# Kernel tuning notes

Measured on AMD Instinct MI355X. Metric: run time of the kernel, lower is better.

Reference implementation:

```python
import jax, jax.numpy as jnp
import numpy as np

B, S, D = 4, 4096, 1024
EPS_LN = 1e-5
EPS_REC = 1e-8


def _layernorm(x, g, b):
    mu = jnp.mean(x, axis=-1, keepdims=True)
    var = jnp.mean((x - mu) ** 2, axis=-1, keepdims=True)
    return (x - mu) * jax.lax.rsqrt(var + EPS_LN) * g + b


def setup_inputs() -> dict:
    key = jax.random.key(0)
    ks = jax.random.split(key, 8)
    scale = 1.0 / np.sqrt(D)
    return {
        "x": jax.random.normal(ks[0], (B, S, D), dtype=jnp.float32),
        "x_prev": jax.random.normal(ks[1], (B, S, D), dtype=jnp.float32),
        "mu": jnp.float32(0.5),
        "decay_w": jax.random.uniform(ks[2], (D, 1), jnp.float32, -scale, scale),
        "decay_b": jnp.zeros((1,), jnp.float32),
        "ln1_g": jnp.ones((D,), jnp.float32),
        "ln1_b": jnp.zeros((D,), jnp.float32),
        "Wr_w": jax.random.uniform(ks[3], (D, D), jnp.float32, -scale, scale),
        "Wr_b": jnp.zeros((D,), jnp.float32),
        "Wv_w": jax.random.uniform(ks[4], (D, D), jnp.float32, -scale, scale),
        "Wv_b": jnp.zeros((D,), jnp.float32),
        "ln2_g": jnp.ones((D,), jnp.float32),
        "ln2_b": jnp.zeros((D,), jnp.float32),
    }


def reference(x, x_prev, mu, decay_w, decay_b, ln1_g, ln1_b,
              Wr_w, Wr_b, Wv_w, Wv_b, ln2_g, ln2_b):
    # Shift (token-mix by scalar mu)
    shifted = mu * x + (1.0 - mu) * x_prev  # [B,S,D]

    # SequenceMergingSeq with C = V = W = shifted
    decay = jax.nn.sigmoid(jnp.einsum("bsd,do->bso", shifted, decay_w) + decay_b)  # [B,S,1]
    e = jnp.exp(shifted)                       # [B,S,D]
    ea = jnp.sum(e, axis=-1, keepdims=True)    # [B,S,1]
    ev = e * shifted                           # [B,S,D]

    def step(carry, inp):
        a, b = carry
        d_t, ea_t, ev_t = inp
        a = d_t * a + ea_t            # [B,1]
        b = d_t * b + ev_t            # [B,D]
        return (a, b), b / (a + EPS_REC)

    init = (jnp.zeros((B, 1), shifted.dtype), jnp.zeros((B, D), shifted.dtype))
    xs = (jnp.swapaxes(decay, 0, 1), jnp.swapaxes(ea, 0, 1), jnp.swapaxes(ev, 0, 1))
    _, out_sbd = jax.lax.scan(step, init, xs)  # [S,B,D]
    merged = _layernorm(jnp.swapaxes(out_sbd, 0, 1), ln1_g, ln1_b)  # [B,S,D]

    # StateCoupling
    gate = jax.nn.sigmoid(jnp.einsum("bsd,ed->bse", merged, Wr_w) + Wr_b)
    value = jnp.einsum("bsd,ed->bse", merged, Wv_w) + Wv_b
    coupled = _layernorm(gate * value, ln2_g, ln2_b)

    return shifted + coupled
```

## Files before the change

### kernel.cpp

```cpp
#include <hip/hip_runtime.h>

#define BATCH 4
#define SEQ   4096
#define DIM   1024
#define NCH   512
#define CHK   8
#define NROWS (BATCH*SEQ)
#define NKT   32

typedef __attribute__((ext_vector_type(4))) float f32x4;
typedef __attribute__((ext_vector_type(8))) short shortx8;
typedef __attribute__((ext_vector_type(4))) short shortx4;

static __device__ __forceinline__ unsigned short f2bf(float f){
    unsigned int u = __float_as_uint(f);
    u += 0x7FFFu + ((u >> 16) & 1u);
    return (unsigned short)(u >> 16);
}
static __device__ __forceinline__ float bf2f(unsigned short h){
    return __uint_as_float(((unsigned int)h) << 16);
}
static __device__ __forceinline__ float sigmoidf_fast(float x){
    return 1.0f / (1.0f + __expf(-x));
}
static __device__ __forceinline__ shortx4 pack4(f32x4 s){
    shortx4 o;
    o.x = (short)f2bf(s.x); o.y = (short)f2bf(s.y);
    o.z = (short)f2bf(s.z); o.w = (short)f2bf(s.w);
    return o;
}
static __device__ __forceinline__ f32x4 unpack4(shortx4 s){
    f32x4 o;
    o.x = bf2f((unsigned short)s.x); o.y = bf2f((unsigned short)s.y);
    o.z = bf2f((unsigned short)s.z); o.w = bf2f((unsigned short)s.w);
    return o;
}

__global__ __launch_bounds__(256) void k_shift_scan(
    const float* __restrict__ X, const float* __restrict__ XP,
    const float* __restrict__ mu_p, const float* __restrict__ dw,
    const float* __restrict__ db_p,
    const float* __restrict__ Wr, const float* __restrict__ Wv,
    unsigned short* __restrict__ Wcat,
    unsigned short* __restrict__ shifted,
    unsigned short* __restrict__ b_local, float* __restrict__ a_local,
    float* __restrict__ cumP)
{
    const int tid  = threadIdx.x;

    if (blockIdx.x >= 512){
        const int pb = blockIdx.x - 512;
        #pragma unroll 4
        for (int i = 0; i < 32; ++i){
            const int n = pb*32 + i;
            const int grp = n >> 5, r = n & 31;
            const float* src = (r < 16) ? (Wr + (size_t)(grp*16 + r)*DIM)
                                        : (Wv + (size_t)(grp*16 + (r-16))*DIM);
            f32x4 v = reinterpret_cast<const f32x4*>(src)[tid];
            reinterpret_cast<shortx4*>(Wcat)[n*256 + tid] = pack4(v);
        }
        return;
    }

    const int lane = tid & 63;
    const int wid  = tid >> 6;
    const int cid  = blockIdx.x*4 + wid;
    const int batch = cid >> 9;
    const int chunk = cid & (NCH-1);
    const int row0  = batch*SEQ + chunk*CHK;

    const float mu = mu_p[0];
    const float om = 1.0f - mu;
    const float db = db_p[0];

    const f32x4* dwv = reinterpret_cast<const f32x4*>(dw);
    const f32x4 w0 = dwv[lane], w1 = dwv[64+lane], w2 = dwv[128+lane], w3 = dwv[192+lane];

    f32x4 b0 = {0,0,0,0}, b1 = {0,0,0,0}, b2 = {0,0,0,0}, b3 = {0,0,0,0};
    float a_run = 0.f, cp = 1.f;

    const f32x4* Xv  = reinterpret_cast<const f32x4*>(X);
    const f32x4* XPv = reinterpret_cast<const f32x4*>(XP);
    shortx4* BL = reinterpret_cast<shortx4*>(b_local);
    shortx4* SH = reinterpret_cast<shortx4*>(shifted);

    for (int r = 0; r < CHK; ++r){
        const int row = row0 + r;
        const int rb  = row*(DIM/4);

        f32x4 x0 = Xv[rb+lane],     x1 = Xv[rb+64+lane],
              x2 = Xv[rb+128+lane], x3 = Xv[rb+192+lane];
        f32x4 p0 = XPv[rb+lane],     p1 = XPv[rb+64+lane],
              p2 = XPv[rb+128+lane], p3 = XPv[rb+192+lane];
        f32x4 s0 = mu*x0 + om*p0, s1 = mu*x1 + om*p1;
        f32x4 s2 = mu*x2 + om*p2, s3 = mu*x3 + om*p3;

        SH[rb+lane]     = pack4(s0);
        SH[rb+64+lane]  = pack4(s1);
        SH[rb+128+lane] = pack4(s2);
        SH[rb+192+lane] = pack4(s3);

        float dot = s0.x*w0.x + s0.y*w0.y + s0.z*w0.z + s0.w*w0.w
                  + s1.x*w1.x + s1.y*w1.y + s1.z*w1.z + s1.w*w1.w
                  + s2.x*w2.x + s2.y*w2.y + s2.z*w2.z + s2.w*w2.w
                  + s3.x*w3.x + s3.y*w3.y + s3.z*w3.z + s3.w*w3.w;

        f32x4 e0, e1, e2, e3;
        e0.x=__expf(s0.x); e0.y=__expf(s0.y); e0.z=__expf(s0.z); e0.w=__expf(s0.w);
        e1.x=__expf(s1.x); e1.y=__expf(s1.y); e1.z=__expf(s1.z); e1.w=__expf(s1.w);
        e2.x=__expf(s2.x); e2.y=__expf(s2.y); e2.z=__expf(s2.z); e2.w=__expf(s2.w);
        e3.x=__expf(s3.x); e3.y=__expf(s3.y); e3.z=__expf(s3.z); e3.w=__expf(s3.w);
        float ea = e0.x+e0.y+e0.z+e0.w + e1.x+e1.y+e1.z+e1.w
                 + e2.x+e2.y+e2.z+e2.w + e3.x+e3.y+e3.z+e3.w;

        #pragma unroll
        for (int off = 1; off < 64; off <<= 1){
            dot += __shfl_xor(dot, off, 64);
            ea  += __shfl_xor(ea,  off, 64);
        }

        const float dt = sigmoidf_fast(dot + db);
        a_run = dt*a_run + ea;
        cp   *= dt;
        b0 = dt*b0 + e0*s0;  b1 = dt*b1 + e1*s1;
        b2 = dt*b2 + e2*s2;  b3 = dt*b3 + e3*s3;

        BL[rb+lane]     = pack4(b0);
        BL[rb+64+lane]  = pack4(b1);
        BL[rb+128+lane] = pack4(b2);
        BL[rb+192+lane] = pack4(b3);
        if (lane == 0){ a_local[row] = a_run; cumP[row] = cp; }
    }
}

__global__ __launch_bounds__(64) void k_combine(
    const unsigned short* __restrict__ b_local, const float* __restrict__ a_local,
    const float* __restrict__ cumP,
    float* __restrict__ carryA, unsigned short* __restrict__ carryB)
{
    const int batch = blockIdx.x >> 2;
    const int dseg  = blockIdx.x & 3;
    const int tid = threadIdx.x;
    const int d0 = dseg*256 + tid*4;

    __shared__ float sP[NCH], sA[NCH];
    for (int c = tid; c < NCH; c += 64){
        const int er = batch*SEQ + c*CHK + (CHK-1);
        sP[c] = cumP[er];
        sA[c] = a_local[er];
    }
    __syncthreads();

    const unsigned short* bl = b_local + (size_t)batch*SEQ*DIM + d0;
    unsigned short* cB = carryB + (size_t)batch*NCH*DIM + d0;
    const bool wA = (dseg == 0 && tid == 0);
    float* cAp = carryA + batch*NCH;

    shortx4 pf[16];
    #pragma unroll
    for (int i = 0; i < 16; ++i)
        pf[i] = *reinterpret_cast<const shortx4*>(bl + (i*CHK + CHK-1)*DIM);

    f32x4 cb = {0,0,0,0};
    float ca = 0.f;

    for (int cc = 0; cc < NCH; cc += 16){
        const bool more = (cc + 16 < NCH);
        #pragma unroll
        for (int k = 0; k < 16; ++k){
            const int c = cc + k;
            f32x4 v = unpack4(pf[k]);
            if (more)
                pf[k] = *reinterpret_cast<const shortx4*>(bl + ((c+16)*CHK + CHK-1)*DIM);
            *reinterpret_cast<shortx4*>(cB + (size_t)c*DIM) = pack4(cb);
            if (wA) cAp[c] = ca;
            const float p = sP[c];
            cb = p*cb + v;
            ca = p*ca + sA[c];
        }
    }
}

__global__ __launch_bounds__(256) void k_fix_ln1(
    const unsigned short* __restrict__ b_local, const float* __restrict__ a_local,
    const float* __restrict__ cumP, const float* __restrict__ carryA,
    const unsigned short* __restrict__ carryB,
    const float* __restrict__ g1, const float* __restrict__ bb1,
    unsigned short* __restrict__ merged)
{
    const int tid = threadIdx.x, lane = tid & 63, wid = tid >> 6;
    const int row = blockIdx.x*4 + wid;
    const int batch = row >> 12;
    const int c = (row & (SEQ-1)) >> 3;

    const float cpv = cumP[row];
    const float a = a_local[row] + cpv * carryA[batch*NCH + c];
    const float inv_a = 1.0f / (a + 1e-8f);

    const shortx4* BL = reinterpret_cast<const shortx4*>(b_local) + (size_t)row*256;
    const shortx4* CB = reinterpret_cast<const shortx4*>(carryB) + (size_t)(batch*NCH + c)*256;

    f32x4 o[4];
    float s = 0.f, s2 = 0.f;
    #pragma unroll
    for (int j = 0; j < 4; ++j){
        f32x4 bl = unpack4(BL[j*64 + lane]);
        f32x4 cb = unpack4(CB[j*64 + lane]);
        f32x4 v = (bl + cpv*cb) * inv_a;
        o[j] = v;
        s  += v.x+v.y+v.z+v.w;
        s2 += v.x*v.x + v.y*v.y + v.z*v.z + v.w*v.w;
    }
    #pragma unroll
    for (int off = 1; off < 64; off <<= 1){
        s  += __shfl_xor(s,  off, 64);
        s2 += __shfl_xor(s2, off, 64);
    }
    const float mean = s * (1.0f/DIM);
    const float rstd = rsqrtf(s2*(1.0f/DIM) - mean*mean + 1e-5f);
    shortx4* MG = reinterpret_cast<shortx4*>(merged) + (size_t)row*256;
    #pragma unroll
    for (int j = 0; j < 4; ++j){
        f32x4 gg = reinterpret_cast<const f32x4*>(g1)[j*64 + lane];
        f32x4 bb = reinterpret_cast<const f32x4*>(bb1)[j*64 + lane];
        MG[j*64 + lane] = pack4((o[j] - mean)*rstd*gg + bb);
    }
}

typedef __attribute__((address_space(3))) unsigned int lds_uint;
typedef __attribute__((address_space(1))) unsigned int glob_uint;
static __device__ __forceinline__ void gload16(const unsigned short* g, char* l){
    __builtin_amdgcn_global_load_lds((const glob_uint*)g, (lds_uint*)l, 16, 0, 0);
}
#define SBAR() do { __builtin_amdgcn_sched_barrier(0); __builtin_amdgcn_s_barrier(); __builtin_amdgcn_sched_barrier(0); } while(0)
#define LGKM0() do { asm volatile("s_waitcnt lgkmcnt(0)" ::: "memory"); __builtin_amdgcn_sched_barrier(0); } while(0)
#define VMC(n)  do { asm volatile("s_waitcnt vmcnt(" #n ")" ::: "memory"); __builtin_amdgcn_sched_barrier(0); } while(0)
#define LDSE 136

__global__ __launch_bounds__(256, 1) void k_gemm(
    const unsigned short* __restrict__ A,
    const unsigned short* __restrict__ Bt,
    const float* __restrict__ rbias, const float* __restrict__ vbias,
    unsigned short* __restrict__ gv)
{
    __shared__ __align__(16) char lds[69632];
    const int tid  = threadIdx.x;
    const int lane = tid & 63;
    const int wid  = tid >> 6;
    const int wm   = wid >> 1;
    const int wn   = wid & 1;

    const int bid  = blockIdx.x;
    const int wgid = (bid & 7)*64 + (bid >> 3);
    const int mt = wgid >> 3, nt = wgid & 7;
    const int m0 = mt*256, n0 = nt*256;

    const int rin = lane >> 2;
    const int scg = (lane & 3) ^ (((lane >> 5) & 1) << 1);
    const unsigned short* gA = A  + (size_t)(m0 + wid*64 + rin)*DIM + scg*8;
    const unsigned short* gB = Bt + (size_t)(n0 + wid*64 + rin)*DIM + scg*8;

    const int fr = lane & 15, fq = lane >> 4;
    const int soff = fr*64 + ((fq*16) ^ ((fr & 8) ? 32 : 0));

    f32x4 acc[8][8];
    #pragma unroll
    for (int i = 0; i < 8; ++i)
        #pragma unroll
        for (int j = 0; j < 8; ++j) acc[i][j] = (f32x4){0,0,0,0};

    auto STAGE = [&](int tk){
        char* base = lds + (tk & 1)*32768;
        const unsigned short* sa = gA + tk*32;
        const unsigned short* sb = gB + tk*32;
        #pragma unroll
        for (int s = 0; s < 4; ++s){
            gload16(sa + (size_t)(s*16)*DIM, base + (wid*4 + s)*1024);
            gload16(sb + (size_t)(s*16)*DIM, base + 16384 + (wid*4 + s)*1024);
        }
    };

    shortx8 af[8], bf[8];

    STAGE(0); STAGE(1);
    VMC(8);
    SBAR();

    for (int T = 0; T < NKT; ++T){
        const char* base = lds + (T & 1)*32768;

        #pragma unroll
        for (int m = 0; m < 8; ++m)
            af[m] = *reinterpret_cast<const shortx8*>(base + (wm*8 + m)*1024 + soff);
        #pragma unroll
        for (int n = 0; n < 8; ++n)
            bf[n] = *reinterpret_cast<const shortx8*>(base + 16384 + (wn*8 + n)*1024 + soff);
        LGKM0();
        SBAR();

        if (T + 2 < NKT) STAGE(T + 2);

        __builtin_amdgcn_s_setprio(1);
        #pragma unroll
        for (int m = 0; m < 8; ++m)
            #pragma unroll
            for (int n = 0; n < 8; ++n)
                acc[m][n] = __builtin_amdgcn_mfma_f32_16x16x32_bf16(af[m], bf[n], acc[m][n], 0, 0, 0);
        __builtin_amdgcn_s_setprio(0);

        if (T + 1 < NKT){
            if (T + 2 < NKT) { VMC(8); } else { VMC(0); }
            SBAR();
        }
    }

    #pragma unroll
    for (int half = 0; half < 2; ++half){
        __syncthreads();
        unsigned short* ep = reinterpret_cast<unsigned short*>(lds);
        if (wm == half){
            #pragma unroll
            for (int j = 0; j < 4; ++j){
                const int ecol = wn*64 + j*16 + fr;
                const float rbe = rbias[nt*128 + ecol];
                const float vbe = vbias[nt*128 + ecol];
                #pragma unroll
                for (int m = 0; m < 8; ++m){
                    const int rbase = m*16 + fq*4;
                    f32x4 ga = acc[m][2*j], va = acc[m][2*j+1];
                    #pragma unroll
                    for (int q = 0; q < 4; ++q){
                        const float g = sigmoidf_fast(ga[q] + rbe);
                        ep[(rbase + q)*LDSE + ecol] = f2bf(g*(va[q] + vbe));
                    }
                }
            }
        }
        __syncthreads();
        #pragma unroll
        for (int p = 0; p < 8; ++p){
            const int r  = p*16 + (tid >> 4);
            const int c8 = tid & 15;
            shortx8 val = *reinterpret_cast<const shortx8*>(&ep[r*LDSE + c8*8]);
            *reinterpret_cast<shortx8*>(
                &gv[(size_t)(m0 + half*128 + r)*DIM + nt*128 + c8*8]) = val;
        }
    }
}

__global__ __launch_bounds__(256) void k_ln2_res(
    const unsigned short* __restrict__ gvb, const unsigned short* __restrict__ shifted,
    const float* __restrict__ g2, const float* __restrict__ b2,
    float* __restrict__ out)
{
    const int tid = threadIdx.x, lane = tid & 63, wid = tid >> 6;
    const int row = blockIdx.x*4 + wid;

    const shortx4* GV = reinterpret_cast<const shortx4*>(gvb) + (size_t)row*256;
    const shortx4* SH = reinterpret_cast<const shortx4*>(shifted) + (size_t)row*256;

    f32x4 v[4];
    float s = 0.f, s2 = 0.f;
    #pragma unroll
    for (int j = 0; j < 4; ++j){
        f32x4 x = unpack4(GV[j*64 + lane]);
        v[j] = x;
        s  += x.x+x.y+x.z+x.w;
        s2 += x.x*x.x + x.y*x.y + x.z*x.z + x.w*x.w;
    }
    #pragma unroll
    for (int off = 1; off < 64; off <<= 1){
        s  += __shfl_xor(s,  off, 64);
        s2 += __shfl_xor(s2, off, 64);
    }
    const float mean = s * (1.0f/DIM);
    const float rstd = rsqrtf(s2*(1.0f/DIM) - mean*mean + 1e-5f);
    f32x4* O = reinterpret_cast<f32x4*>(out) + (size_t)row*256;
    #pragma unroll
    for (int j = 0; j < 4; ++j){
        f32x4 gg = reinterpret_cast<const f32x4*>(g2)[j*64 + lane];
        f32x4 bb = reinterpret_cast<const f32x4*>(b2)[j*64 + lane];
        f32x4 sh = unpack4(SH[j*64 + lane]);
        O[j*64 + lane] = sh + (v[j] - mean)*rstd*gg + bb;
    }
}

extern "C" void kernel_launch(void* const* d_in, const int* in_sizes, int n_in,
                              void* d_out, int out_size, void* d_ws, size_t ws_size,
                              hipStream_t stream)
{
    (void)in_sizes; (void)n_in; (void)out_size; (void)ws_size;
    const float* x     = (const float*)d_in[0];
    const float* xprev = (const float*)d_in[1];
    const float* mu    = (const float*)d_in[2];
    const float* dw    = (const float*)d_in[3];
    const float* db    = (const float*)d_in[4];
    const float* ln1g  = (const float*)d_in[5];
    const float* ln1b  = (const float*)d_in[6];
    const float* Wr    = (const float*)d_in[7];
    const float* Wrb   = (const float*)d_in[8];
    const float* Wv    = (const float*)d_in[9];
    const float* Wvb   = (const float*)d_in[10];
    const float* ln2g  = (const float*)d_in[11];
    const float* ln2b  = (const float*)d_in[12];
    float* out = (float*)d_out;

    char* ws = (char*)d_ws;
    size_t off = 0;
    auto alloc = [&](size_t bytes) -> void* {
        void* p = ws + off;
        off += (bytes + 255) & ~(size_t)255;
        return p;
    };
    unsigned short* shifted = (unsigned short*)alloc((size_t)NROWS*DIM*2);
    unsigned short* b_local = (unsigned short*)alloc((size_t)NROWS*DIM*2);
    unsigned short* merged  = (unsigned short*)alloc((size_t)NROWS*DIM*2);
    unsigned short* carryB  = (unsigned short*)alloc((size_t)BATCH*NCH*DIM*2);
    unsigned short* Wcat    = (unsigned short*)alloc((size_t)2048*1024*2);
    float* a_local          = (float*)alloc((size_t)NROWS*4);
    float* cumP             = (float*)alloc((size_t)NROWS*4);
    float* carryA           = (float*)alloc((size_t)BATCH*NCH*4);
    unsigned short* gvbuf   = b_local;

    hipLaunchKernelGGL(k_shift_scan, dim3(576),  dim3(256), 0, stream,
                       x, xprev, mu, dw, db, Wr, Wv, Wcat, shifted, b_local, a_local, cumP);
    hipLaunchKernelGGL(k_combine,    dim3(16),   dim3(64),  0, stream,
                       b_local, a_local, cumP, carryA, carryB);
    hipLaunchKernelGGL(k_fix_ln1,    dim3(4096), dim3(256), 0, stream,
                       b_local, a_local, cumP, carryA, carryB, ln1g, ln1b, merged);
    hipLaunchKernelGGL(k_gemm,       dim3(512),  dim3(256), 0, stream,
                       merged, Wcat, Wrb, Wvb, gvbuf);
    hipLaunchKernelGGL(k_ln2_res,    dim3(4096), dim3(256), 0, stream,
                       gvbuf, shifted, ln2g, ln2b, out);
}
```

Before: 227.1 us.

## Retile GEMM to 256x128 tiles with 8 waves and triple-buffered LDS

Restructures the fused gate/value GEMM from 256x256 tiles with 4 waves and 8x8 MFMA accumulators per wave to 256x128 tiles with 8 waves and 4x4 accumulators, on a grid of 1024 blocks of 512 threads. Replaces the double-buffered LDS pipeline with a three-stage ring, issuing the next stage before the fragment reads, which removes one barrier per k-step. The epilogue is rewritten as a single pass over the whole tile. The aim is more parallel blocks and fewer accumulator registers for better occupancy and latency hiding, at the cost of lower per-wave arithmetic intensity and more global traffic for the A and B tiles.

```diff
diff --git a/kernel.cpp b/kernel.cpp
--- a/kernel.cpp
+++ b/kernel.cpp
@@ -235,15 +235,15 @@
 #define SBAR() do { __builtin_amdgcn_sched_barrier(0); __builtin_amdgcn_s_barrier(); __builtin_amdgcn_sched_barrier(0); } while(0)
 #define LGKM0() do { asm volatile("s_waitcnt lgkmcnt(0)" ::: "memory"); __builtin_amdgcn_sched_barrier(0); } while(0)
 #define VMC(n)  do { asm volatile("s_waitcnt vmcnt(" #n ")" ::: "memory"); __builtin_amdgcn_sched_barrier(0); } while(0)
-#define LDSE 136
-
-__global__ __launch_bounds__(256, 1) void k_gemm(
+#define LDSE 72
+
+__global__ __launch_bounds__(512, 4) void k_gemm(
     const unsigned short* __restrict__ A,
     const unsigned short* __restrict__ Bt,
     const float* __restrict__ rbias, const float* __restrict__ vbias,
     unsigned short* __restrict__ gv)
 {
-    __shared__ __align__(16) char lds[69632];
+    __shared__ __align__(16) char lds[73728];
     const int tid  = threadIdx.x;
     const int lane = tid & 63;
     const int wid  = tid >> 6;
@@ -251,100 +251,94 @@
     const int wn   = wid & 1;
 
     const int bid  = blockIdx.x;
-    const int wgid = (bid & 7)*64 + (bid >> 3);
-    const int mt = wgid >> 3, nt = wgid & 7;
-    const int m0 = mt*256, n0 = nt*256;
+    const int wgid = (bid & 7)*128 + (bid >> 3);
+    const int mt = wgid >> 4, nt = wgid & 15;
+    const int m0 = mt*256, n0 = nt*128;
 
     const int rin = lane >> 2;
     const int scg = (lane & 3) ^ (((lane >> 5) & 1) << 1);
-    const unsigned short* gA = A  + (size_t)(m0 + wid*64 + rin)*DIM + scg*8;
-    const unsigned short* gB = Bt + (size_t)(n0 + wid*64 + rin)*DIM + scg*8;
+    const unsigned short* pA = A  + (size_t)(m0 + rin)*DIM + scg*8;
+    const unsigned short* pB = Bt + (size_t)(n0 + rin)*DIM + scg*8;
 
     const int fr = lane & 15, fq = lane >> 4;
     const int soff = fr*64 + ((fq*16) ^ ((fr & 8) ? 32 : 0));
 
-    f32x4 acc[8][8];
-    #pragma unroll
-    for (int i = 0; i < 8; ++i)
-        #pragma unroll
-        for (int j = 0; j < 8; ++j) acc[i][j] = (f32x4){0,0,0,0};
-
-    auto STAGE = [&](int tk){
-        char* base = lds + (tk & 1)*32768;
-        const unsigned short* sa = gA + tk*32;
-        const unsigned short* sb = gB + tk*32;
-        #pragma unroll
-        for (int s = 0; s < 4; ++s){
-            gload16(sa + (size_t)(s*16)*DIM, base + (wid*4 + s)*1024);
-            gload16(sb + (size_t)(s*16)*DIM, base + 16384 + (wid*4 + s)*1024);
+    f32x4 acc[4][4];
+    #pragma unroll
+    for (int i = 0; i < 4; ++i)
+        #pragma unroll
+        for (int j = 0; j < 4; ++j) acc[i][j] = (f32x4){0,0,0,0};
+
+    auto STAGE = [&](int T){
+        if (T >= NKT) return;
+        char* base = lds + (T % 3)*24576;
+        #pragma unroll
+        for (int s = 0; s < 3; ++s){
+            const int sub = wid*3 + s;
+            const unsigned short* src = (sub < 16)
+                ? pA + (size_t)(sub*16)*DIM + T*32
+                : pB + (size_t)((sub-16)*16)*DIM + T*32;
+            char* dst = base + ((sub < 16) ? sub*1024 : 16384 + (sub-16)*1024);
+            gload16(src, dst);
         }
     };
 
-    shortx8 af[8], bf[8];
+    shortx8 af[4], bf[4];
 
     STAGE(0); STAGE(1);
-    VMC(8);
+    VMC(3);
     SBAR();
 
     for (int T = 0; T < NKT; ++T){
-        const char* base = lds + (T & 1)*32768;
-
-        #pragma unroll
-        for (int m = 0; m < 8; ++m)
-            af[m] = *reinterpret_cast<const shortx8*>(base + (wm*8 + m)*1024 + soff);
-        #pragma unroll
-        for (int n = 0; n < 8; ++n)
-            bf[n] = *reinterpret_cast<const shortx8*>(base + 16384 + (wn*8 + n)*1024 + soff);
+        const char* base = lds + (T % 3)*24576;
+
+        STAGE(T + 2);
+
+        #pragma unroll
+        for (int mf = 0; mf < 4; ++mf)
+            af[mf] = *reinterpret_cast<const shortx8*>(base + (wm*4 + mf)*1024 + soff);
+        #pragma unroll
+        for (int nf = 0; nf < 4; ++nf)
+            bf[nf] = *reinterpret_cast<const shortx8*>(base + 16384 + (wn*4 + nf)*1024 + soff);
         LGKM0();
-        SBAR();
-
-        if (T + 2 < NKT) STAGE(T + 2);
 
         __builtin_amdgcn_s_setprio(1);
         #pragma unroll
-        for (int m = 0; m < 8; ++m)
+        for (int mf = 0; mf < 4; ++mf)
             #pragma unroll
-            for (int n = 0; n < 8; ++n)
-                acc[m][n] = __builtin_amdgcn_mfma_f32_16x16x32_bf16(af[m], bf[n], acc[m][n], 0, 0, 0);
+            for (int nf = 0; nf < 4; ++nf)
+                acc[mf][nf] = __builtin_amdgcn_mfma_f32_16x16x32_bf16(af[mf], bf[nf], acc[mf][nf], 0, 0, 0);
         __builtin_amdgcn_s_setprio(0);
 
-        if (T + 1 < NKT){
-            if (T + 2 < NKT) { VMC(8); } else { VMC(0); }
-            SBAR();
-        }
-    }
-
-    #pragma unroll
-    for (int half = 0; half < 2; ++half){
-        __syncthreads();
-        unsigned short* ep = reinterpret_cast<unsigned short*>(lds);
-        if (wm == half){
+        if (T + 2 < NKT)      { VMC(3); SBAR(); }
+        else if (T + 1 < NKT) { VMC(0); SBAR(); }
+    }
+
+    __syncthreads();
+    unsigned short* ep = reinterpret_cast<unsigned short*>(lds);
+    #pragma unroll
+    for (int p = 0; p < 2; ++p){
+        const int el = wn*32 + p*16 + fr;
+        const float rbe = rbias[nt*64 + el];
+        const float vbe = vbias[nt*64 + el];
+        #pragma unroll
+        for (int mf = 0; mf < 4; ++mf){
+            const int rbase = wm*64 + mf*16 + fq*4;
+            f32x4 ga = acc[mf][2*p], va = acc[mf][2*p+1];
             #pragma unroll
-            for (int j = 0; j < 4; ++j){
-                const int ecol = wn*64 + j*16 + fr;
-                const float rbe = rbias[nt*128 + ecol];
-                const float vbe = vbias[nt*128 + ecol];
-                #pragma unroll
-                for (int m = 0; m < 8; ++m){
-                    const int rbase = m*16 + fq*4;
-                    f32x4 ga = acc[m][2*j], va = acc[m][2*j+1];
-                    #pragma unroll
-                    for (int q = 0; q < 4; ++q){
-                        const float g = sigmoidf_fast(ga[q] + rbe);
-                        ep[(rbase + q)*LDSE + ecol] = f2bf(g*(va[q] + vbe));
-                    }
-                }
+            for (int q = 0; q < 4; ++q){
+                const float g = sigmoidf_fast(ga[q] + rbe);
+                ep[(rbase + q)*LDSE + el] = f2bf(g*(va[q] + vbe));
             }
         }
-        __syncthreads();
-        #pragma unroll
-        for (int p = 0; p < 8; ++p){
-            const int r  = p*16 + (tid >> 4);
-            const int c8 = tid & 15;
-            shortx8 val = *reinterpret_cast<const shortx8*>(&ep[r*LDSE + c8*8]);
-            *reinterpret_cast<shortx8*>(
-                &gv[(size_t)(m0 + half*128 + r)*DIM + nt*128 + c8*8]) = val;
-        }
+    }
+    __syncthreads();
+    #pragma unroll
+    for (int p = 0; p < 4; ++p){
+        const int r  = p*64 + (tid >> 3);
+        const int c8 = tid & 7;
+        shortx8 val = *reinterpret_cast<const shortx8*>(&ep[r*LDSE + c8*8]);
+        *reinterpret_cast<shortx8*>(&gv[(size_t)(m0 + r)*DIM + nt*64 + c8*8]) = val;
     }
 }
 
@@ -428,7 +422,7 @@
                        b_local, a_local, cumP, carryA, carryB);
     hipLaunchKernelGGL(k_fix_ln1,    dim3(4096), dim3(256), 0, stream,
                        b_local, a_local, cumP, carryA, carryB, ln1g, ln1b, merged);
-    hipLaunchKernelGGL(k_gemm,       dim3(512),  dim3(256), 0, stream,
+    hipLaunchKernelGGL(k_gemm,       dim3(1024), dim3(512), 0, stream,
                        merged, Wcat, Wrb, Wvb, gvbuf);
     hipLaunchKernelGGL(k_ln2_res,    dim3(4096), dim3(256), 0, stream,
                        gvbuf, shifted, ln2g, ln2b, out);
```

Result: faster. 209.3 us (-7.9%).
